# Kernel optimization log

Hardware: AMD Instinct MI355X
Metric: run time of the kernel (lower is better)

The kernel has to match this reference:

```python
import jax, jax.numpy as jnp
import numpy as np

N, K, D = 131072, 512, 512
ALPHA = 1.0


def setup_inputs() -> dict:
    key = jax.random.key(0)
    kx, kc = jax.random.split(key)
    x = jax.random.normal(kx, (N, D), dtype=jnp.float32)
    # Xavier uniform for clusters: limit = sqrt(6/(K+D))
    limit = float(np.sqrt(6.0 / (K + D)))
    clusters = jax.random.uniform(kc, (K, D), dtype=jnp.float32, minval=-limit, maxval=limit)
    return {"x": x, "clusters": clusters}


def reference(x, clusters):
    # mathematically equal to sum((x[:,None,:]-c[None,:,:])**2, axis=2)
    x2 = jnp.sum(x * x, axis=1, keepdims=True)            # (N, 1)
    c2 = jnp.sum(clusters * clusters, axis=1)             # (K,)
    d2 = x2 + c2[None, :] - 2.0 * (x @ clusters.T)        # (N, K)
    d2 = jnp.maximum(d2, 0.0)  # guard tiny negatives from cancellation
    q = 1.0 / (1.0 + d2 / ALPHA)
    q = q ** ((ALPHA + 1.0) / 2.0)
    q = q / jnp.sum(q, axis=1, keepdims=True)
    return q
```

## Files before the change

### kernel.cpp

```cpp
#include <hip/hip_runtime.h>
#include <hip/hip_bf16.h>
#include <stdint.h>

#define N_ROWS 131072
#define K_CL   512
#define D_DIM  512
#define M_TILE 64
#define BK     32
#define STEPS  (D_DIM / BK)

typedef __attribute__((ext_vector_type(8))) short short8;
typedef __attribute__((ext_vector_type(4))) float f32x4;

__device__ __forceinline__ unsigned short f2bf(float f) {
  union { float f; unsigned u; } v; v.f = f;
  unsigned r = v.u + 0x7fffu + ((v.u >> 16) & 1u);
  return (unsigned short)(r >> 16);
}

__device__ __forceinline__ void glds16(const void* g, void* l) {
  __builtin_amdgcn_global_load_lds(
      (const __attribute__((address_space(1))) void*)g,
      (__attribute__((address_space(3))) void*)l, 16, 0, 0);
}

__global__ void prep_clusters(const float* __restrict__ c,
                              unsigned short* __restrict__ cb,
                              float* __restrict__ c2) {
  const int b = blockIdx.x;
  const int l = threadIdx.x;
  const float* row = c + (size_t)b * D_DIM;
  float s = 0.f;
  #pragma unroll
  for (int i = 0; i < 2; ++i) {
    const int col = i * 256 + l * 4;
    float4 v = *(const float4*)(row + col);
    s += v.x * v.x + v.y * v.y + v.z * v.z + v.w * v.w;
    *(ushort4*)(cb + (size_t)b * D_DIM + col) =
        make_ushort4(f2bf(v.x), f2bf(v.y), f2bf(v.z), f2bf(v.w));
  }
  #pragma unroll
  for (int m = 1; m < 64; m <<= 1) s += __shfl_xor(s, m);
  if (l == 0) c2[b] = s;
}

__global__ __launch_bounds__(256, 2)
void cluster_main(const float* __restrict__ x,
                  const unsigned short* __restrict__ cb,
                  const float* __restrict__ c2,
                  float* __restrict__ out) {
  __shared__ short As[M_TILE * 40];
  __shared__ short Bs[4 * 128 * BK];
  __shared__ float c2s[K_CL];
  __shared__ float x2s[M_TILE];
  __shared__ float rowsum[4][M_TILE];
  __shared__ float rinv[M_TILE];

  const int t = threadIdx.x;
  const int w = t >> 6;
  const int l = t & 63;
  const int row0 = blockIdx.x * M_TILE;

  c2s[t] = c2[t];
  c2s[t + 256] = c2[t + 256];

  f32x4 acc[4][8];
  #pragma unroll
  for (int i = 0; i < 4; ++i)
    #pragma unroll
    for (int j = 0; j < 8; ++j) acc[i][j] = (f32x4){0.f, 0.f, 0.f, 0.f};

  const int rowA = t >> 3;
  const int rowB = rowA + 32;
  const int kc   = (t & 7) * 4;
  float ssA = 0.f, ssB = 0.f;

  short* BsW = &Bs[w * 128 * BK];

  for (int kk = 0; kk < STEPS; ++kk) {
    __syncthreads();

    const float4 va = *(const float4*)(x + (size_t)(row0 + rowA) * D_DIM + kk * BK + kc);
    const float4 vb = *(const float4*)(x + (size_t)(row0 + rowB) * D_DIM + kk * BK + kc);

    #pragma unroll
    for (int i = 0; i < 8; ++i) {
      const int cg = w * 128 + i * 16 + (l >> 2);
      const unsigned short* g = cb + (size_t)cg * D_DIM + kk * BK + (l & 3) * 8;
      glds16(g, BsW + i * 16 * BK);
    }

    ssA += va.x * va.x + va.y * va.y + va.z * va.z + va.w * va.w;
    ssB += vb.x * vb.x + vb.y * vb.y + vb.z * vb.z + vb.w * vb.w;
    *(ushort4*)&As[rowA * 40 + kc] =
        make_ushort4(f2bf(va.x), f2bf(va.y), f2bf(va.z), f2bf(va.w));
    *(ushort4*)&As[rowB * 40 + kc] =
        make_ushort4(f2bf(vb.x), f2bf(vb.y), f2bf(vb.z), f2bf(vb.w));

    __syncthreads();

    short8 a[4];
    #pragma unroll
    for (int rt = 0; rt < 4; ++rt)
      a[rt] = *(const short8*)&As[(rt * 16 + (l & 15)) * 40 + (l >> 4) * 8];

    #pragma unroll
    for (int ct = 0; ct < 8; ++ct) {
      short8 b = *(const short8*)&BsW[(ct * 16 + (l & 15)) * BK + (l >> 4) * 8];
      #pragma unroll
      for (int rt = 0; rt < 4; ++rt)
        acc[rt][ct] = __builtin_amdgcn_mfma_f32_16x16x32_bf16(a[rt], b, acc[rt][ct], 0, 0, 0);
    }
  }

  float s1 = ssA, s2 = ssB;
  s1 += __shfl_xor(s1, 1); s1 += __shfl_xor(s1, 2); s1 += __shfl_xor(s1, 4);
  s2 += __shfl_xor(s2, 1); s2 += __shfl_xor(s2, 2); s2 += __shfl_xor(s2, 4);
  if ((t & 7) == 0) { x2s[rowA] = s1; x2s[rowB] = s2; }
  __syncthreads();

  const int lg = l >> 4;
  const int ln = l & 15;

  float xr[4][4];
  #pragma unroll
  for (int rt = 0; rt < 4; ++rt)
    #pragma unroll
    for (int r = 0; r < 4; ++r) xr[rt][r] = x2s[rt * 16 + lg * 4 + r];
  float cv[8];
  #pragma unroll
  for (int ct = 0; ct < 8; ++ct) cv[ct] = c2s[w * 128 + ct * 16 + ln];

  float rp[4][4];
  #pragma unroll
  for (int rt = 0; rt < 4; ++rt)
    #pragma unroll
    for (int r = 0; r < 4; ++r) rp[rt][r] = 0.f;

  #pragma unroll
  for (int rt = 0; rt < 4; ++rt)
    #pragma unroll
    for (int ct = 0; ct < 8; ++ct) {
      f32x4 s = acc[rt][ct], q;
      #pragma unroll
      for (int r = 0; r < 4; ++r) {
        float d2 = xr[rt][r] + cv[ct] - 2.f * s[r];
        d2 = fmaxf(d2, 0.f);
        float qq = __builtin_amdgcn_rcpf(1.f + d2);
        q[r] = qq;
        rp[rt][r] += qq;
      }
      acc[rt][ct] = q;
    }

  #pragma unroll
  for (int m = 1; m < 16; m <<= 1)
    #pragma unroll
    for (int rt = 0; rt < 4; ++rt)
      #pragma unroll
      for (int r = 0; r < 4; ++r) rp[rt][r] += __shfl_xor(rp[rt][r], m);

  if (ln == 0)
    #pragma unroll
    for (int rt = 0; rt < 4; ++rt)
      #pragma unroll
      for (int r = 0; r < 4; ++r)
        rowsum[w][rt * 16 + lg * 4 + r] = rp[rt][r];
  __syncthreads();

  if (t < M_TILE) {
    float tot = rowsum[0][t] + rowsum[1][t] + rowsum[2][t] + rowsum[3][t];
    rinv[t] = __builtin_amdgcn_rcpf(tot);
  }
  __syncthreads();

  float ri[4][4];
  #pragma unroll
  for (int rt = 0; rt < 4; ++rt)
    #pragma unroll
    for (int r = 0; r < 4; ++r) ri[rt][r] = rinv[rt * 16 + lg * 4 + r];

  #pragma unroll
  for (int rt = 0; rt < 4; ++rt)
    #pragma unroll
    for (int ct = 0; ct < 8; ++ct)
      #pragma unroll
      for (int r = 0; r < 4; ++r)
        out[(size_t)(row0 + rt * 16 + lg * 4 + r) * K_CL + w * 128 + ct * 16 + ln] =
            acc[rt][ct][r] * ri[rt][r];
}

extern "C" void kernel_launch(void* const* d_in, const int* in_sizes, int n_in,
                              void* d_out, int out_size, void* d_ws, size_t ws_size,
                              hipStream_t stream) {
  const float* x        = (const float*)d_in[0];
  const float* clusters = (const float*)d_in[1];
  float* out = (float*)d_out;

  unsigned short* cb = (unsigned short*)d_ws;
  float* c2 = (float*)((char*)d_ws + (size_t)K_CL * D_DIM * sizeof(unsigned short));

  prep_clusters<<<K_CL, 64, 0, stream>>>(clusters, cb, c2);
  cluster_main<<<N_ROWS / M_TILE, 256, 0, stream>>>(x, cb, c2, out);
}
```

Measured before the change: 501.4 us.

## Pre-pack cluster B fragments, load directly to registers, double-buffer A, nontemporal stores

Cluster bf16 data is repacked into MFMA fragment order by a new kernel, so each wave loads its B operands straight from global (L2-resident) into registers instead of staging through LDS with global_load_lds. The A tile is double-buffered in LDS with the next x slice prefetched into registers, which removes one barrier per K step. Output stores become nontemporal to avoid polluting cache with the large write stream. This trades LDS traffic and syncs for more global/L2 load traffic per wave and higher register pressure.

```diff
diff --git a/kernel.cpp b/kernel.cpp
--- a/kernel.cpp
+++ b/kernel.cpp
@@ -18,15 +18,7 @@
   return (unsigned short)(r >> 16);
 }
 
-__device__ __forceinline__ void glds16(const void* g, void* l) {
-  __builtin_amdgcn_global_load_lds(
-      (const __attribute__((address_space(1))) void*)g,
-      (__attribute__((address_space(3))) void*)l, 16, 0, 0);
-}
-
-__global__ void prep_clusters(const float* __restrict__ c,
-                              unsigned short* __restrict__ cb,
-                              float* __restrict__ c2) {
+__global__ void prep_c2(const float* __restrict__ c, float* __restrict__ c2) {
   const int b = blockIdx.x;
   const int l = threadIdx.x;
   const float* row = c + (size_t)b * D_DIM;
@@ -36,21 +28,33 @@
     const int col = i * 256 + l * 4;
     float4 v = *(const float4*)(row + col);
     s += v.x * v.x + v.y * v.y + v.z * v.z + v.w * v.w;
-    *(ushort4*)(cb + (size_t)b * D_DIM + col) =
-        make_ushort4(f2bf(v.x), f2bf(v.y), f2bf(v.z), f2bf(v.w));
   }
   #pragma unroll
   for (int m = 1; m < 64; m <<= 1) s += __shfl_xor(s, m);
   if (l == 0) c2[b] = s;
 }
 
+__global__ void pack_b(const float* __restrict__ c, unsigned short* __restrict__ pb) {
+  const int bid = blockIdx.x;
+  const int c16 = bid & 31;
+  const int kk  = bid >> 5;
+  const int l   = threadIdx.x;
+  const int row = c16 * 16 + (l & 15);
+  const int k0  = kk * 32 + (l >> 4) * 8;
+  float4 v0 = *(const float4*)(c + (size_t)row * D_DIM + k0);
+  float4 v1 = *(const float4*)(c + (size_t)row * D_DIM + k0 + 4);
+  ushort4 u0 = make_ushort4(f2bf(v0.x), f2bf(v0.y), f2bf(v0.z), f2bf(v0.w));
+  ushort4 u1 = make_ushort4(f2bf(v1.x), f2bf(v1.y), f2bf(v1.z), f2bf(v1.w));
+  *(ushort4*)(pb + (size_t)(bid * 64 + l) * 8)     = u0;
+  *(ushort4*)(pb + (size_t)(bid * 64 + l) * 8 + 4) = u1;
+}
+
 __global__ __launch_bounds__(256, 2)
 void cluster_main(const float* __restrict__ x,
-                  const unsigned short* __restrict__ cb,
+                  const unsigned short* __restrict__ pb,
                   const float* __restrict__ c2,
                   float* __restrict__ out) {
-  __shared__ short As[M_TILE * 40];
-  __shared__ short Bs[4 * 128 * BK];
+  __shared__ short As[2][M_TILE * 40];
   __shared__ float c2s[K_CL];
   __shared__ float x2s[M_TILE];
   __shared__ float rowsum[4][M_TILE];
@@ -75,42 +79,45 @@
   const int kc   = (t & 7) * 4;
   float ssA = 0.f, ssB = 0.f;
 
-  short* BsW = &Bs[w * 128 * BK];
-
+  const float* xA = x + (size_t)(row0 + rowA) * D_DIM + kc;
+  const float* xB = x + (size_t)(row0 + rowB) * D_DIM + kc;
+
+  float4 va = *(const float4*)(xA);
+  float4 vb = *(const float4*)(xB);
+
+  int cur = 0;
   for (int kk = 0; kk < STEPS; ++kk) {
-    __syncthreads();
-
-    const float4 va = *(const float4*)(x + (size_t)(row0 + rowA) * D_DIM + kk * BK + kc);
-    const float4 vb = *(const float4*)(x + (size_t)(row0 + rowB) * D_DIM + kk * BK + kc);
-
-    #pragma unroll
-    for (int i = 0; i < 8; ++i) {
-      const int cg = w * 128 + i * 16 + (l >> 2);
-      const unsigned short* g = cb + (size_t)cg * D_DIM + kk * BK + (l & 3) * 8;
-      glds16(g, BsW + i * 16 * BK);
-    }
-
     ssA += va.x * va.x + va.y * va.y + va.z * va.z + va.w * va.w;
     ssB += vb.x * vb.x + vb.y * vb.y + vb.z * vb.z + vb.w * vb.w;
-    *(ushort4*)&As[rowA * 40 + kc] =
+    *(ushort4*)&As[cur][rowA * 40 + kc] =
         make_ushort4(f2bf(va.x), f2bf(va.y), f2bf(va.z), f2bf(va.w));
-    *(ushort4*)&As[rowB * 40 + kc] =
+    *(ushort4*)&As[cur][rowB * 40 + kc] =
         make_ushort4(f2bf(vb.x), f2bf(vb.y), f2bf(vb.z), f2bf(vb.w));
 
+    if (kk + 1 < STEPS) {
+      va = *(const float4*)(xA + (kk + 1) * BK);
+      vb = *(const float4*)(xB + (kk + 1) * BK);
+    }
+
+    short8 b[8];
+    #pragma unroll
+    for (int ct = 0; ct < 8; ++ct)
+      b[ct] = *(const short8*)(pb + ((size_t)(kk * 32 + w * 8 + ct) * 64 + l) * 8);
+
     __syncthreads();
 
     short8 a[4];
     #pragma unroll
     for (int rt = 0; rt < 4; ++rt)
-      a[rt] = *(const short8*)&As[(rt * 16 + (l & 15)) * 40 + (l >> 4) * 8];
-
-    #pragma unroll
-    for (int ct = 0; ct < 8; ++ct) {
-      short8 b = *(const short8*)&BsW[(ct * 16 + (l & 15)) * BK + (l >> 4) * 8];
+      a[rt] = *(const short8*)&As[cur][(rt * 16 + (l & 15)) * 40 + (l >> 4) * 8];
+
+    #pragma unroll
+    for (int ct = 0; ct < 8; ++ct)
       #pragma unroll
       for (int rt = 0; rt < 4; ++rt)
-        acc[rt][ct] = __builtin_amdgcn_mfma_f32_16x16x32_bf16(a[rt], b, acc[rt][ct], 0, 0, 0);
-    }
+        acc[rt][ct] = __builtin_amdgcn_mfma_f32_16x16x32_bf16(a[rt], b[ct], acc[rt][ct], 0, 0, 0);
+
+    cur ^= 1;
   }
 
   float s1 = ssA, s2 = ssB;
@@ -186,8 +193,9 @@
     for (int ct = 0; ct < 8; ++ct)
       #pragma unroll
       for (int r = 0; r < 4; ++r)
-        out[(size_t)(row0 + rt * 16 + lg * 4 + r) * K_CL + w * 128 + ct * 16 + ln] =
-            acc[rt][ct][r] * ri[rt][r];
+        __builtin_nontemporal_store(
+            acc[rt][ct][r] * ri[rt][r],
+            &out[(size_t)(row0 + rt * 16 + lg * 4 + r) * K_CL + w * 128 + ct * 16 + ln]);
 }
 
 extern "C" void kernel_launch(void* const* d_in, const int* in_sizes, int n_in,
@@ -197,9 +205,10 @@
   const float* clusters = (const float*)d_in[1];
   float* out = (float*)d_out;
 
-  unsigned short* cb = (unsigned short*)d_ws;
+  unsigned short* pbuf = (unsigned short*)d_ws;
   float* c2 = (float*)((char*)d_ws + (size_t)K_CL * D_DIM * sizeof(unsigned short));
 
-  prep_clusters<<<K_CL, 64, 0, stream>>>(clusters, cb, c2);
-  cluster_main<<<N_ROWS / M_TILE, 256, 0, stream>>>(x, cb, c2, out);
-}
+  prep_c2<<<K_CL, 64, 0, stream>>>(clusters, c2);
+  pack_b<<<STEPS * 32, 64, 0, stream>>>(clusters, pbuf);
+  cluster_main<<<N_ROWS / M_TILE, 256, 0, stream>>>(x, pbuf, c2, out);
+}
```

Result: no change. 498.7 us (-0.5%).
